# Kernel tuning notes

Hardware: AMD Instinct MI355X
Metric: run time of the kernel (lower is better)

The kernel has to match this reference:

```python
import jax, jax.numpy as jnp
import numpy as np

NUM_RAYS = 4096
NUM_SAMPLES = 64
NUM_IMPORTANCE = 64
UPSAMPLE_STEPS = 4
HIDDEN = 128
SAMPLE_DIST = 2.0 / NUM_SAMPLES
COS_ANNEAL_RATIO = 0.0


def sdf_fn(params, pts):
    # pts: [P,3] -> sdf: [P,1]  (stand-in for sdf_network.get_sdf_vals)
    W1, b1, W2, b2, W3, b3 = params
    h = jax.nn.softplus(pts @ W1 + b1)
    h = jax.nn.softplus(h @ W2 + b2)
    return h @ W3 + b3


def sdf_grad(params, pts):
    # gradient of sdf w.r.t. points, [P,3] (stand-in for sdf_network.gradient)
    return jax.grad(lambda p: sdf_fn(params, p).sum())(pts)


def sample_pdf(bins, weights, n_samples):
    # deterministic inverse-transform sampling (det=True branch)
    weights = weights + 1e-5
    pdf = weights / jnp.sum(weights, axis=-1, keepdims=True)
    cdf = jnp.cumsum(pdf, axis=-1)
    cdf = jnp.concatenate([jnp.zeros_like(cdf[..., :1]), cdf], axis=-1)  # [N,S]
    u = jnp.linspace(0.5 / n_samples, 1.0 - 0.5 / n_samples, n_samples, dtype=cdf.dtype)
    u = jnp.broadcast_to(u, cdf.shape[:-1] + (n_samples,))
    inds = jax.vmap(lambda c, uu: jnp.searchsorted(c, uu, side='right'))(cdf, u)
    below = jnp.maximum(inds - 1, 0)
    above = jnp.minimum(inds, cdf.shape[-1] - 1)
    cdf_b = jnp.take_along_axis(cdf, below, axis=-1)
    cdf_a = jnp.take_along_axis(cdf, above, axis=-1)
    bins_b = jnp.take_along_axis(bins, below, axis=-1)
    bins_a = jnp.take_along_axis(bins, above, axis=-1)
    denom = cdf_a - cdf_b
    denom = jnp.where(denom < 1e-5, jnp.ones_like(denom), denom)
    t = (u - cdf_b) / denom
    return bins_b + t * (bins_a - bins_b)


def upsample(rays_o, rays_d, z_vals, sdf, n_importance, inv_s):
    N, S = z_vals.shape
    pts = rays_o[:, None, :] + rays_d[:, None, :] * z_vals[..., None]  # [N,S,3]
    radius = jnp.linalg.norm(pts, axis=-1)
    inside_sphere = ((radius[:, :-1] < 1.0) | (radius[:, 1:] < 1.0)).astype(z_vals.dtype)
    prev_sdf, next_sdf = sdf[:, :-1], sdf[:, 1:]
    prev_z, next_z = z_vals[:, :-1], z_vals[:, 1:]
    mid_sdf = (prev_sdf + next_sdf) * 0.5
    cos_val = (next_sdf - prev_sdf) / (next_z - prev_z + 1e-5)
    prev_cos = jnp.concatenate([jnp.zeros((N, 1), z_vals.dtype), cos_val[:, :-1]], axis=-1)
    cos_val = jnp.minimum(prev_cos, cos_val)
    cos_val = jnp.clip(cos_val, -1000.0, 0.0) * inside_sphere
    dist = next_z - prev_z
    prev_cdf = jax.nn.sigmoid((mid_sdf - cos_val * dist * 0.5) * inv_s)
    next_cdf = jax.nn.sigmoid((mid_sdf + cos_val * dist * 0.5) * inv_s)
    alpha = (prev_cdf - next_cdf + 1e-5) / (prev_cdf + 1e-5)
    trans = jnp.cumprod(jnp.concatenate([jnp.ones((N, 1), z_vals.dtype), 1.0 - alpha + 1e-7], axis=-1), axis=-1)[:, :-1]
    weights = alpha * trans
    return sample_pdf(z_vals, weights, n_importance)


def cat_z_vals(params, rays_o, rays_d, z_vals, new_z_vals, sdf, last):
    N = z_vals.shape[0]
    z_cat = jnp.concatenate([z_vals, new_z_vals], axis=-1)
    order = jnp.argsort(z_cat, axis=-1)
    z_sorted = jnp.take_along_axis(z_cat, order, axis=-1)
    if not last:
        pts = rays_o[:, None, :] + rays_d[:, None, :] * new_z_vals[..., None]
        new_sdf = sdf_fn(params, pts.reshape(-1, 3)).reshape(N, new_z_vals.shape[-1])
        sdf = jnp.take_along_axis(jnp.concatenate([sdf, new_sdf], axis=-1), order, axis=-1)
    return z_sorted, sdf


def render_depth(params, variance, rays_o, rays_d, sample_dist, z_vals):
    N, S = z_vals.shape
    dists = z_vals[..., 1:] - z_vals[..., :-1]
    dists = jnp.concatenate([dists, jnp.full((N, 1), sample_dist, z_vals.dtype)], axis=-1)
    mid_z = z_vals + dists * 0.5
    pts = (rays_o[:, None, :] + rays_d[:, None, :] * mid_z[..., None]).reshape(-1, 3)
    dirs = jnp.broadcast_to(rays_d[:, None, :], (N, S, 3)).reshape(-1, 3)
    sdf = sdf_fn(params, pts)              # [P,1]
    gradients = sdf_grad(params, pts)      # [P,3]
    inv_s = jnp.clip(jnp.exp(10.0 * variance), 1e-6, 1e6)
    true_cos = jnp.sum(dirs * gradients, axis=-1, keepdims=True)
    iter_cos = -(jax.nn.relu(-true_cos * 0.5 + 0.5) * (1.0 - COS_ANNEAL_RATIO)
                 + jax.nn.relu(-true_cos) * COS_ANNEAL_RATIO)
    d = dists.reshape(-1, 1)
    prev_cdf = jax.nn.sigmoid((sdf - iter_cos * d * 0.5) * inv_s)
    next_cdf = jax.nn.sigmoid((sdf + iter_cos * d * 0.5) * inv_s)
    alpha = jnp.clip((prev_cdf - next_cdf + 1e-5) / (prev_cdf + 1e-5), 0.0, 1.0).reshape(N, S)
    trans = jnp.cumprod(jnp.concatenate([jnp.ones((N, 1), z_vals.dtype), 1.0 - alpha + 1e-7], axis=-1), axis=-1)[:, :-1]
    weights = alpha * trans
    depths = jnp.sum(weights * z_vals, axis=-1)
    return depths, gradients


def setup_inputs():
    key = jax.random.key(0)
    ks = jax.random.split(key, 8)
    rays_o = 0.1 * jax.random.normal(ks[0], (NUM_RAYS, 3), jnp.float32)
    rd = jax.random.normal(ks[1], (NUM_RAYS, 3), jnp.float32)
    rays_d = rd / jnp.linalg.norm(rd, axis=-1, keepdims=True)
    near = 0.3 + 0.2 * jax.random.uniform(ks[2], (NUM_RAYS, 1), jnp.float32)
    far = near + 1.5
    W1 = jax.random.normal(ks[3], (3, HIDDEN), jnp.float32) / np.sqrt(3.0)
    W2 = jax.random.normal(ks[4], (HIDDEN, HIDDEN), jnp.float32) / np.sqrt(HIDDEN)
    W3 = jax.random.normal(ks[5], (HIDDEN, 1), jnp.float32) / np.sqrt(HIDDEN)
    b1 = jnp.zeros((HIDDEN,), jnp.float32)
    b2 = jnp.zeros((HIDDEN,), jnp.float32)
    b3 = jnp.zeros((1,), jnp.float32)
    variance = jnp.asarray(0.3, jnp.float32)
    return {"rays_o": rays_o, "rays_d": rays_d, "near": near, "far": far,
            "W1": W1, "b1": b1, "W2": W2, "b2": b2, "W3": W3, "b3": b3,
            "variance": variance}


def reference(rays_o, rays_d, near, far, W1, b1, W2, b2, W3, b3, variance):
    params = (W1, b1, W2, b2, W3, b3)
    N = rays_o.shape[0]
    z = jnp.linspace(0.0, 1.0, NUM_SAMPLES, dtype=jnp.float32)
    z_vals = near + (far - near) * z[None, :]  # [N,S0]
    # importance sampling (torch.no_grad block)
    pts = rays_o[:, None, :] + rays_d[:, None, :] * z_vals[..., None]
    sdf = sdf_fn(params, pts.reshape(-1, 3)).reshape(N, NUM_SAMPLES)
    n_imp = NUM_IMPORTANCE // UPSAMPLE_STEPS
    for i in range(UPSAMPLE_STEPS):
        new_z = upsample(rays_o, rays_d, z_vals, sdf, n_imp, 64.0 * (2 ** i))
        z_vals, sdf = cat_z_vals(params, rays_o, rays_d, z_vals, new_z, sdf,
                                 last=(i + 1 == UPSAMPLE_STEPS))
    z_vals = jax.lax.stop_gradient(z_vals)
    return render_depth(params, variance, rays_o, rays_d, SAMPLE_DIST, z_vals)
```

## Files before the change

### kernel.cpp

```cpp
#include <hip/hip_runtime.h>
#include <math.h>

#define HID 128
#define NRAYS 4096
#define TP 64

typedef __bf16 bf16x8 __attribute__((ext_vector_type(8)));
typedef float f32x4 __attribute__((ext_vector_type(4)));
typedef unsigned int uint32x4 __attribute__((ext_vector_type(4)));

union frag_u { bf16x8 v; uint32x4 q; };

__device__ __forceinline__ unsigned f2bf(float f){
  unsigned u = __float_as_uint(f);
  u += 0x7FFFu + ((u >> 16) & 1u);
  return u >> 16;
}
__device__ __forceinline__ float bf2f(unsigned h){
  return __uint_as_float(h << 16);
}
__device__ __forceinline__ float sp_f(float x){
  return fmaxf(x, 0.0f) + log1pf(expf(-fabsf(x)));
}
__device__ __forceinline__ float sp_fast(float x){
  float e = __expf(-fabsf(x));
  return fmaxf(x, 0.0f) + __logf(1.0f + e);
}
__device__ __forceinline__ float sg_fast(float x){
  float e = __expf(-fabsf(x));
  float r = __builtin_amdgcn_rcpf(1.0f + e);
  return (x >= 0.0f ? 1.0f : e) * r;
}
__device__ __forceinline__ float sg_f(float x){
  return 1.0f / (1.0f + expf(-x));
}
__device__ __forceinline__ f32x4 splat4(float x){
  f32x4 v = {x, x, x, x};
  return v;
}

#define SW(p,k) ((((p)*HID) + (k)) ^ (((p)&7)<<3))

__global__ void k_make_frags(const float* __restrict__ W2,
    unsigned short* __restrict__ w2fh,  unsigned short* __restrict__ w2fl,
    unsigned short* __restrict__ w2tfh, unsigned short* __restrict__ w2tfl){
  int idx = blockIdx.x*256 + threadIdx.x;
  if (idx >= 4096) return;
  int which = idx >> 11;
  int f    = (idx >> 6) & 31;
  int lane = idx & 63;
  int kc = f >> 3, tg = f & 7;
  int lg = lane >> 4, lr = lane & 15;
  unsigned short* dh = which ? w2tfh : w2fh;
  unsigned short* dl = which ? w2tfl : w2fl;
  int base = (f*64 + lane)*8;
  #pragma unroll
  for (int e = 0; e < 8; e++){
    int a = 32*kc + 8*lg + e;
    int b = 16*tg + lr;
    float v = which ? W2[b*HID + a] : W2[a*HID + b];
    unsigned hi = f2bf(v);
    dh[base+e] = (unsigned short)hi;
    dl[base+e] = (unsigned short)f2bf(v - bf2f(hi));
  }
}

__global__ void k_make_frags3(const float* __restrict__ W2,
    unsigned short* __restrict__ dh, unsigned short* __restrict__ dm,
    unsigned short* __restrict__ dl){
  int idx = blockIdx.x*256 + threadIdx.x;
  if (idx >= 2048) return;
  int f    = idx >> 6;
  int lane = idx & 63;
  int kc = f >> 3, tg = f & 7;
  int lg = lane >> 4, lr = lane & 15;
  int base = (f*64 + lane)*8;
  #pragma unroll
  for (int e = 0; e < 8; e++){
    int a = 32*kc + 8*lg + e;
    int b = 16*tg + lr;
    float v = W2[a*HID + b];
    unsigned hi = f2bf(v);
    float rm = v - bf2f(hi);
    unsigned md = f2bf(rm);
    dh[base+e] = (unsigned short)hi;
    dm[base+e] = (unsigned short)md;
    dl[base+e] = (unsigned short)f2bf(rm - bf2f(md));
  }
}

__global__ void k_init(const float* __restrict__ rays_o, const float* __restrict__ rays_d,
                       const float* __restrict__ nearv, const float* __restrict__ farv,
                       float* __restrict__ z_buf, float* __restrict__ pts){
  int idx = blockIdx.x*256 + threadIdx.x;
  if (idx >= NRAYS*64) return;
  int ray = idx >> 6, j = idx & 63;
  float nr = nearv[ray];
  float z = nr + (farv[ray] - nr) * ((float)j / 63.0f);
  z_buf[ray*128 + j] = z;
  pts[idx*3+0] = rays_o[ray*3+0] + rays_d[ray*3+0]*z;
  pts[idx*3+1] = rays_o[ray*3+1] + rays_d[ray*3+1]*z;
  pts[idx*3+2] = rays_o[ray*3+2] + rays_d[ray*3+2]*z;
}

__global__ __launch_bounds__(256, 3) void k_mlp_fwd_t(
    const float* __restrict__ pts,
    const float* __restrict__ W1, const float* __restrict__ b1,
    const float* __restrict__ b2,
    const float* __restrict__ W3, const float* __restrict__ b3,
    const unsigned short* __restrict__ w2h, const unsigned short* __restrict__ w2m,
    const unsigned short* __restrict__ w2l,
    float* __restrict__ sdf_out)
{
  __shared__ unsigned short sHi[64*HID];
  __shared__ unsigned short sMi[64*HID];
  __shared__ unsigned short sLo[64*HID];
  __shared__ float sRed[4][64];

  const int tid = threadIdx.x;
  const int l   = tid & 63;
  const int wv  = __builtin_amdgcn_readfirstlane(tid >> 6);
  const int lg  = l >> 4;
  const int lr  = l & 15;
  const int q0  = blockIdx.x * 64;
  const int kb  = 32*wv;

  const float x0 = pts[(q0+l)*3+0];
  const float x1 = pts[(q0+l)*3+1];
  const float x2 = pts[(q0+l)*3+2];

  #pragma unroll
  for (int g = 0; g < 4; g++){
    unsigned hw[4], mw[4], lw[4];
    #pragma unroll
    for (int e2 = 0; e2 < 4; e2++){
      unsigned hpk[2], mpk[2], lpk[2];
      #pragma unroll
      for (int t = 0; t < 2; t++){
        int k = kb + 8*g + 2*e2 + t;
        float pre = b1[k];
        pre = fmaf(x0, W1[k],       pre);
        pre = fmaf(x1, W1[HID+k],   pre);
        pre = fmaf(x2, W1[2*HID+k], pre);
        float h = sp_fast(pre);
        unsigned hi = f2bf(h);
        float rm = h - bf2f(hi);
        unsigned md = f2bf(rm);
        hpk[t] = hi; mpk[t] = md;
        lpk[t] = f2bf(rm - bf2f(md));
      }
      hw[e2] = hpk[0] | (hpk[1] << 16);
      mw[e2] = mpk[0] | (mpk[1] << 16);
      lw[e2] = lpk[0] | (lpk[1] << 16);
    }
    uint32x4 hq = {hw[0], hw[1], hw[2], hw[3]};
    uint32x4 mq = {mw[0], mw[1], mw[2], mw[3]};
    uint32x4 lq = {lw[0], lw[1], lw[2], lw[3]};
    *(uint32x4*)&sHi[SW(l, kb + 8*g)] = hq;
    *(uint32x4*)&sMi[SW(l, kb + 8*g)] = mq;
    *(uint32x4*)&sLo[SW(l, kb + 8*g)] = lq;
  }
  __syncthreads();

  f32x4 acc[4][2], accC[4][2];
  {
    const float b2a = b2[kb + lr];
    const float b2b = b2[kb + 16 + lr];
    #pragma unroll
    for (int mt = 0; mt < 4; mt++){
      acc[mt][0]  = splat4(b2a);
      acc[mt][1]  = splat4(b2b);
      accC[mt][0] = splat4(0.0f);
      accC[mt][1] = splat4(0.0f);
    }
  }
  #pragma unroll
  for (int kc = 0; kc < 4; kc++){
    frag_u bh0, bm0, bl0, bh1, bm1, bl1;
    const int f0 = ((kc*8 + 2*wv + 0)*64 + l)*8;
    const int f1 = ((kc*8 + 2*wv + 1)*64 + l)*8;
    bh0.q = *(const uint32x4*)(w2h + f0);
    bm0.q = *(const uint32x4*)(w2m + f0);
    bl0.q = *(const uint32x4*)(w2l + f0);
    bh1.q = *(const uint32x4*)(w2h + f1);
    bm1.q = *(const uint32x4*)(w2m + f1);
    bl1.q = *(const uint32x4*)(w2l + f1);
    const int kk = 32*kc + 8*lg;
    #pragma unroll
    for (int mt = 0; mt < 4; mt++){
      frag_u ah, am, al;
      ah.q = *(const uint32x4*)&sHi[SW(16*mt + lr, kk)];
      am.q = *(const uint32x4*)&sMi[SW(16*mt + lr, kk)];
      al.q = *(const uint32x4*)&sLo[SW(16*mt + lr, kk)];
      accC[mt][0] = __builtin_amdgcn_mfma_f32_16x16x32_bf16(ah.v, bl0.v, accC[mt][0], 0,0,0);
      accC[mt][0] = __builtin_amdgcn_mfma_f32_16x16x32_bf16(am.v, bm0.v, accC[mt][0], 0,0,0);
      accC[mt][0] = __builtin_amdgcn_mfma_f32_16x16x32_bf16(al.v, bh0.v, accC[mt][0], 0,0,0);
      accC[mt][0] = __builtin_amdgcn_mfma_f32_16x16x32_bf16(ah.v, bm0.v, accC[mt][0], 0,0,0);
      accC[mt][0] = __builtin_amdgcn_mfma_f32_16x16x32_bf16(am.v, bh0.v, accC[mt][0], 0,0,0);
      acc[mt][0]  = __builtin_amdgcn_mfma_f32_16x16x32_bf16(ah.v, bh0.v, acc[mt][0],  0,0,0);
      accC[mt][1] = __builtin_amdgcn_mfma_f32_16x16x32_bf16(ah.v, bl1.v, accC[mt][1], 0,0,0);
      accC[mt][1] = __builtin_amdgcn_mfma_f32_16x16x32_bf16(am.v, bm1.v, accC[mt][1], 0,0,0);
      accC[mt][1] = __builtin_amdgcn_mfma_f32_16x16x32_bf16(al.v, bh1.v, accC[mt][1], 0,0,0);
      accC[mt][1] = __builtin_amdgcn_mfma_f32_16x16x32_bf16(ah.v, bm1.v, accC[mt][1], 0,0,0);
      accC[mt][1] = __builtin_amdgcn_mfma_f32_16x16x32_bf16(am.v, bh1.v, accC[mt][1], 0,0,0);
      acc[mt][1]  = __builtin_amdgcn_mfma_f32_16x16x32_bf16(ah.v, bh1.v, acc[mt][1],  0,0,0);
    }
  }

  {
    const float w3a = W3[kb + lr];
    const float w3b = W3[kb + 16 + lr];
    #pragma unroll
    for (int mt = 0; mt < 4; mt++){
      float svr[4];
      #pragma unroll
      for (int r = 0; r < 4; r++){
        float pa = acc[mt][0][r] + accC[mt][0][r];
        float pb = acc[mt][1][r] + accC[mt][1][r];
        svr[r] = sp_fast(pa)*w3a + sp_fast(pb)*w3b;
      }
      #pragma unroll
      for (int m = 1; m < 16; m <<= 1){
        svr[0] += __shfl_xor(svr[0], m);
        svr[1] += __shfl_xor(svr[1], m);
        svr[2] += __shfl_xor(svr[2], m);
        svr[3] += __shfl_xor(svr[3], m);
      }
      if (lr == 0){
        sRed[wv][16*mt + 4*lg + 0] = svr[0];
        sRed[wv][16*mt + 4*lg + 1] = svr[1];
        sRed[wv][16*mt + 4*lg + 2] = svr[2];
        sRed[wv][16*mt + 4*lg + 3] = svr[3];
      }
    }
  }
  __syncthreads();
  if (tid < 64)
    sdf_out[q0+tid] = b3[0] + sRed[0][tid] + sRed[1][tid] + sRed[2][tid] + sRed[3][tid];
}

__global__ __launch_bounds__(256, 4) void k_mlp_bwd(
    const float* __restrict__ pts,
    const float* __restrict__ W1, const float* __restrict__ b1,
    const float* __restrict__ b2,
    const float* __restrict__ W3, const float* __restrict__ b3,
    const unsigned short* __restrict__ w2fh,  const unsigned short* __restrict__ w2fl,
    const unsigned short* __restrict__ w2tfh, const unsigned short* __restrict__ w2tfl,
    float* __restrict__ sdf_out, float* __restrict__ grad_out)
{
  __shared__ unsigned short sHi[64*HID];
  __shared__ unsigned short sLo[64*HID];
  __shared__ float sRed[4][64];
  __shared__ float sPts[64][4];
  __shared__ float sGrad[4][64][3];

  const int tid = threadIdx.x;
  const int l   = tid & 63;
  const int wv  = __builtin_amdgcn_readfirstlane(tid >> 6);
  const int lg  = l >> 4;
  const int lr  = l & 15;
  const int q0  = blockIdx.x * 64;
  const int kb  = 32*wv;

  const float x0 = pts[(q0+l)*3+0];
  const float x1 = pts[(q0+l)*3+1];
  const float x2 = pts[(q0+l)*3+2];
  if (wv == 0){ sPts[l][0] = x0; sPts[l][1] = x1; sPts[l][2] = x2; }

  #pragma unroll
  for (int g = 0; g < 4; g++){
    unsigned hw[4], lw[4];
    #pragma unroll
    for (int e2 = 0; e2 < 4; e2++){
      unsigned hpk[2], lpk[2];
      #pragma unroll
      for (int t = 0; t < 2; t++){
        int k = kb + 8*g + 2*e2 + t;
        float pre = b1[k];
        pre = fmaf(x0, W1[k],       pre);
        pre = fmaf(x1, W1[HID+k],   pre);
        pre = fmaf(x2, W1[2*HID+k], pre);
        float h = sp_fast(pre);
        unsigned hi = f2bf(h);
        hpk[t] = hi;
        lpk[t] = f2bf(h - bf2f(hi));
      }
      hw[e2] = hpk[0] | (hpk[1] << 16);
      lw[e2] = lpk[0] | (lpk[1] << 16);
    }
    uint32x4 hq = {hw[0], hw[1], hw[2], hw[3]};
    uint32x4 lq = {lw[0], lw[1], lw[2], lw[3]};
    *(uint32x4*)&sHi[SW(l, kb + 8*g)] = hq;
    *(uint32x4*)&sLo[SW(l, kb + 8*g)] = lq;
  }
  __syncthreads();

  f32x4 acc[4][2];
  {
    const float b2a = b2[kb + lr];
    const float b2b = b2[kb + 16 + lr];
    #pragma unroll
    for (int mt = 0; mt < 4; mt++){
      acc[mt][0] = splat4(b2a);
      acc[mt][1] = splat4(b2b);
    }
  }
  #pragma unroll
  for (int kc = 0; kc < 4; kc++){
    frag_u bh0, bl0, bh1, bl1;
    const int f0 = ((kc*8 + 2*wv + 0)*64 + l)*8;
    const int f1 = ((kc*8 + 2*wv + 1)*64 + l)*8;
    bh0.q = *(const uint32x4*)(w2fh + f0);
    bl0.q = *(const uint32x4*)(w2fl + f0);
    bh1.q = *(const uint32x4*)(w2fh + f1);
    bl1.q = *(const uint32x4*)(w2fl + f1);
    const int kk = 32*kc + 8*lg;
    #pragma unroll
    for (int mt = 0; mt < 4; mt++){
      frag_u ah, al;
      ah.q = *(const uint32x4*)&sHi[SW(16*mt + lr, kk)];
      al.q = *(const uint32x4*)&sLo[SW(16*mt + lr, kk)];
      acc[mt][0] = __builtin_amdgcn_mfma_f32_16x16x32_bf16(ah.v, bh0.v, acc[mt][0], 0,0,0);
      acc[mt][0] = __builtin_amdgcn_mfma_f32_16x16x32_bf16(ah.v, bl0.v, acc[mt][0], 0,0,0);
      acc[mt][0] = __builtin_amdgcn_mfma_f32_16x16x32_bf16(al.v, bh0.v, acc[mt][0], 0,0,0);
      acc[mt][1] = __builtin_amdgcn_mfma_f32_16x16x32_bf16(ah.v, bh1.v, acc[mt][1], 0,0,0);
      acc[mt][1] = __builtin_amdgcn_mfma_f32_16x16x32_bf16(ah.v, bl1.v, acc[mt][1], 0,0,0);
      acc[mt][1] = __builtin_amdgcn_mfma_f32_16x16x32_bf16(al.v, bh1.v, acc[mt][1], 0,0,0);
    }
  }
  __syncthreads();

  {
    const float w3a = W3[kb + lr];
    const float w3b = W3[kb + 16 + lr];
    #pragma unroll
    for (int mt = 0; mt < 4; mt++){
      float svr[4];
      #pragma unroll
      for (int r = 0; r < 4; r++){
        float pa = acc[mt][0][r], pb = acc[mt][1][r];
        svr[r] = sp_fast(pa)*w3a + sp_fast(pb)*w3b;
        int pr = 16*mt + 4*lg + r;
        float ga = sg_fast(pa) * w3a;
        float gb = sg_fast(pb) * w3b;
        unsigned ha = f2bf(ga);
        sHi[SW(pr, kb + lr)]      = (unsigned short)ha;
        sLo[SW(pr, kb + lr)]      = (unsigned short)f2bf(ga - bf2f(ha));
        unsigned hb = f2bf(gb);
        sHi[SW(pr, kb + 16 + lr)] = (unsigned short)hb;
        sLo[SW(pr, kb + 16 + lr)] = (unsigned short)f2bf(gb - bf2f(hb));
      }
      #pragma unroll
      for (int m = 1; m < 16; m <<= 1){
        svr[0] += __shfl_xor(svr[0], m);
        svr[1] += __shfl_xor(svr[1], m);
        svr[2] += __shfl_xor(svr[2], m);
        svr[3] += __shfl_xor(svr[3], m);
      }
      if (lr == 0){
        sRed[wv][16*mt + 4*lg + 0] = svr[0];
        sRed[wv][16*mt + 4*lg + 1] = svr[1];
        sRed[wv][16*mt + 4*lg + 2] = svr[2];
        sRed[wv][16*mt + 4*lg + 3] = svr[3];
      }
    }
  }
  __syncthreads();
  if (tid < 64)
    sdf_out[q0+tid] = b3[0] + sRed[0][tid] + sRed[1][tid] + sRed[2][tid] + sRed[3][tid];

  f32x4 acc2[4][2];
  #pragma unroll
  for (int pt = 0; pt < 4; pt++){
    acc2[pt][0] = splat4(0.0f);
    acc2[pt][1] = splat4(0.0f);
  }
  #pragma unroll
  for (int kcn = 0; kcn < 4; kcn++){
    frag_u ah0, al0, ah1, al1;
    const int f0 = ((kcn*8 + 2*wv + 0)*64 + l)*8;
    const int f1 = ((kcn*8 + 2*wv + 1)*64 + l)*8;
    ah0.q = *(const uint32x4*)(w2tfh + f0);
    al0.q = *(const uint32x4*)(w2tfl + f0);
    ah1.q = *(const uint32x4*)(w2tfh + f1);
    al1.q = *(const uint32x4*)(w2tfl + f1);
    const int nn = 32*kcn + 8*lg;
    #pragma unroll
    for (int pt = 0; pt < 4; pt++){
      frag_u bh, bl;
      bh.q = *(const uint32x4*)&sHi[SW(16*pt + lr, nn)];
      bl.q = *(const uint32x4*)&sLo[SW(16*pt + lr, nn)];
      acc2[pt][0] = __builtin_amdgcn_mfma_f32_16x16x32_bf16(ah0.v, bh.v, acc2[pt][0], 0,0,0);
      acc2[pt][0] = __builtin_amdgcn_mfma_f32_16x16x32_bf16(ah0.v, bl.v, acc2[pt][0], 0,0,0);
      acc2[pt][0] = __builtin_amdgcn_mfma_f32_16x16x32_bf16(al0.v, bh.v, acc2[pt][0], 0,0,0);
      acc2[pt][1] = __builtin_amdgcn_mfma_f32_16x16x32_bf16(ah1.v, bh.v, acc2[pt][1], 0,0,0);
      acc2[pt][1] = __builtin_amdgcn_mfma_f32_16x16x32_bf16(ah1.v, bl.v, acc2[pt][1], 0,0,0);
      acc2[pt][1] = __builtin_amdgcn_mfma_f32_16x16x32_bf16(al1.v, bh.v, acc2[pt][1], 0,0,0);
    }
  }

  {
    float w1a[2][4], w1b[2][4], w1c[2][4], b1v[2][4];
    #pragma unroll
    for (int t = 0; t < 2; t++)
      #pragma unroll
      for (int r = 0; r < 4; r++){
        int k = kb + 16*t + 4*lg + r;
        w1a[t][r] = W1[k]; w1b[t][r] = W1[HID+k]; w1c[t][r] = W1[2*HID+k];
        b1v[t][r] = b1[k];
      }
    #pragma unroll
    for (int pt = 0; pt < 4; pt++){
      const int p = 16*pt + lr;
      const float xx = sPts[p][0], xy = sPts[p][1], xz = sPts[p][2];
      float gx = 0.f, gy = 0.f, gz = 0.f;
      #pragma unroll
      for (int t = 0; t < 2; t++){
        #pragma unroll
        for (int r = 0; r < 4; r++){
          float pre1 = fmaf(xx, w1a[t][r], fmaf(xy, w1b[t][r], fmaf(xz, w1c[t][r], b1v[t][r])));
          float dp = acc2[pt][t][r] * sg_fast(pre1);
          gx = fmaf(w1a[t][r], dp, gx);
          gy = fmaf(w1b[t][r], dp, gy);
          gz = fmaf(w1c[t][r], dp, gz);
        }
      }
      gx += __shfl_xor(gx, 16); gx += __shfl_xor(gx, 32);
      gy += __shfl_xor(gy, 16); gy += __shfl_xor(gy, 32);
      gz += __shfl_xor(gz, 16); gz += __shfl_xor(gz, 32);
      if (lg == 0){
        sGrad[wv][p][0] = gx; sGrad[wv][p][1] = gy; sGrad[wv][p][2] = gz;
      }
    }
  }
  __syncthreads();
  if (tid < 64){
    #pragma unroll
    for (int c = 0; c < 3; c++)
      grad_out[(q0+tid)*3+c] =
        sGrad[0][tid][c] + sGrad[1][tid][c] + sGrad[2][tid][c] + sGrad[3][tid][c];
  }
}

__global__ void k_scatter_init(const float* __restrict__ sdf_tmp, float* __restrict__ sdf_buf){
  int idx = blockIdx.x*256 + threadIdx.x;
  if (idx >= NRAYS*64) return;
  sdf_buf[(idx >> 6)*128 + (idx & 63)] = sdf_tmp[idx];
}
__global__ void k_scatter_new(const float* __restrict__ sdf_tmp, const int* __restrict__ slots,
                              float* __restrict__ sdf_buf){
  int idx = blockIdx.x*256 + threadIdx.x;
  if (idx >= NRAYS*16) return;
  sdf_buf[(idx >> 4)*128 + slots[idx]] = sdf_tmp[idx];
}

__global__ __launch_bounds__(64) void k_upsample(
      const float* __restrict__ rays_o, const float* __restrict__ rays_d,
      float* __restrict__ z_buf, float* __restrict__ sdf_buf,
      float* __restrict__ pts_new, int* __restrict__ slots,
      int S, float inv_s, int last){
  __shared__ float z[128], sd[128], rad[128], cosv[128], alf[128], wv[128], cdf[129], nz[16];
  __shared__ int slt[16];
  const int ray = blockIdx.x;
  const int l   = threadIdx.x;
  const float ox = rays_o[ray*3], oy = rays_o[ray*3+1], oz = rays_o[ray*3+2];
  const float dx = rays_d[ray*3], dy = rays_d[ray*3+1], dz = rays_d[ray*3+2];
  for (int j = l; j < S; j += 64){
    float zz = z_buf[ray*128+j];
    z[j]  = zz;
    sd[j] = sdf_buf[ray*128+j];
    float px = ox+dx*zz, py = oy+dy*zz, pz = oz+dz*zz;
    rad[j] = sqrtf(px*px + py*py + pz*pz);
  }
  __syncthreads();
  for (int j = l; j < S-1; j += 64)
    cosv[j] = (sd[j+1]-sd[j]) / (z[j+1]-z[j] + 1e-5f);
  __syncthreads();
  for (int j = l; j < S-1; j += 64){
    float cv = fminf((j > 0) ? cosv[j-1] : 0.0f, cosv[j]);
    cv = fminf(fmaxf(cv, -1000.0f), 0.0f);
    float inside = (rad[j] < 1.0f || rad[j+1] < 1.0f) ? 1.0f : 0.0f;
    cv *= inside;
    float mid  = 0.5f*(sd[j]+sd[j+1]);
    float dist = z[j+1]-z[j];
    float e = sg_f((mid - cv*dist*0.5f)*inv_s);
    float f = sg_f((mid + cv*dist*0.5f)*inv_s);
    alf[j] = (e - f + 1e-5f) / (e + 1e-5f);
  }
  __syncthreads();
  if (l == 0){
    float T = 1.0f, wsum = 0.0f;
    for (int j = 0; j < S-1; j++){
      float w = alf[j]*T + 1e-5f;
      wv[j] = w; wsum += w;
      T *= (1.0f - alf[j] + 1e-7f);
    }
    cdf[0] = 0.0f;
    float c = 0.0f;
    for (int j = 0; j < S-1; j++){ c += wv[j]/wsum; cdf[j+1] = c; }
  }
  __syncthreads();
  if (l < 16){
    float u = 0.03125f + 0.0625f*(float)l;
    int idx = 0;
    while (idx < S && cdf[idx] <= u) idx++;
    int below = idx - 1; if (below < 0) below = 0;
    int above = (idx < S-1) ? idx : (S-1);
    float cb = cdf[below], ca = cdf[above];
    float den = ca - cb; if (den < 1e-5f) den = 1.0f;
    float t = (u - cb) / den;
    nz[l] = z[below] + t*(z[above] - z[below]);
  }
  __syncthreads();
  if (l == 0){
    int i = S-1, j = 15;
    for (int dst = S+15; dst >= 0; --dst){
      bool takeOld = (j < 0) || (i >= 0 && z[i] > nz[j]);
      if (takeOld){ z[dst] = z[i]; sd[dst] = sd[i]; i--; }
      else        { z[dst] = nz[j]; slt[j] = dst; j--; }
    }
  }
  __syncthreads();
  for (int j = l; j < S+16; j += 64){
    z_buf[ray*128+j]  = z[j];
    sdf_buf[ray*128+j] = sd[j];
  }
  if (!last && l < 16){
    slots[ray*16+l] = slt[l];
    float zz = nz[l];
    pts_new[(ray*16+l)*3+0] = ox + dx*zz;
    pts_new[(ray*16+l)*3+1] = oy + dy*zz;
    pts_new[(ray*16+l)*3+2] = oz + dz*zz;
  }
}

__global__ void k_prep(const float* __restrict__ rays_o, const float* __restrict__ rays_d,
                       const float* __restrict__ z_buf, float* __restrict__ pts){
  int idx = blockIdx.x*256 + threadIdx.x;
  if (idx >= NRAYS*128) return;
  int ray = idx >> 7, s = idx & 127;
  float z = z_buf[idx];
  float d = (s < 127) ? (z_buf[idx+1] - z) : 0.03125f;
  float mid = z + 0.5f*d;
  pts[idx*3+0] = rays_o[ray*3+0] + rays_d[ray*3+0]*mid;
  pts[idx*3+1] = rays_o[ray*3+1] + rays_d[ray*3+1]*mid;
  pts[idx*3+2] = rays_o[ray*3+2] + rays_d[ray*3+2]*mid;
}

__global__ __launch_bounds__(64) void k_render(
    const float* __restrict__ z_buf, const float* __restrict__ sdf_mid,
    const float* __restrict__ rays_d, const float* __restrict__ grad,
    const float* __restrict__ variance, float* __restrict__ depth_out){
  const int ray = blockIdx.x;
  const int l   = threadIdx.x;
  float inv_s = expf(10.0f * variance[0]);
  inv_s = fminf(fmaxf(inv_s, 1e-6f), 1e6f);
  const float dx = rays_d[ray*3], dy = rays_d[ray*3+1], dz = rays_d[ray*3+2];
  const int i0 = ray*128 + 2*l, i1 = i0 + 1;
  const float z0 = z_buf[i0], z1 = z_buf[i1];
  const float zn1 = __shfl_down(z0, 1);
  const float d0 = z1 - z0;
  const float d1 = (l < 63) ? (zn1 - z1) : 0.03125f;
  float a0, a1;
  {
    float sdf = sdf_mid[i0];
    float gx = grad[i0*3], gy = grad[i0*3+1], gz = grad[i0*3+2];
    float tc = dx*gx + dy*gy + dz*gz;
    float ic = -fmaxf(0.5f - 0.5f*tc, 0.0f);
    float e = sg_fast((sdf - ic*d0*0.5f)*inv_s);
    float f = sg_fast((sdf + ic*d0*0.5f)*inv_s);
    a0 = fminf(fmaxf((e - f + 1e-5f) / (e + 1e-5f), 0.0f), 1.0f);
  }
  {
    float sdf = sdf_mid[i1];
    float gx = grad[i1*3], gy = grad[i1*3+1], gz = grad[i1*3+2];
    float tc = dx*gx + dy*gy + dz*gz;
    float ic = -fmaxf(0.5f - 0.5f*tc, 0.0f);
    float e = sg_fast((sdf - ic*d1*0.5f)*inv_s);
    float f = sg_fast((sdf + ic*d1*0.5f)*inv_s);
    a1 = fminf(fmaxf((e - f + 1e-5f) / (e + 1e-5f), 0.0f), 1.0f);
  }
  const float f0 = 1.0f - a0 + 1e-7f;
  const float f1 = 1.0f - a1 + 1e-7f;
  float incl = f0 * f1;
  #pragma unroll
  for (int off = 1; off < 64; off <<= 1){
    float t = __shfl_up(incl, off);
    if (l >= off) incl *= t;
  }
  float P = __shfl_up(incl, 1);
  if (l == 0) P = 1.0f;
  float part = P * (a0*z0 + f0*a1*z1);
  #pragma unroll
  for (int m = 1; m < 64; m <<= 1) part += __shfl_xor(part, m);
  if (l == 0) depth_out[ray] = part;
}

extern "C" void kernel_launch(void* const* d_in, const int* in_sizes, int n_in,
                              void* d_out, int out_size, void* d_ws, size_t ws_size,
                              hipStream_t stream){
  (void)in_sizes; (void)n_in; (void)out_size; (void)ws_size;
  const float* rays_o = (const float*)d_in[0];
  const float* rays_d = (const float*)d_in[1];
  const float* nearv  = (const float*)d_in[2];
  const float* farv   = (const float*)d_in[3];
  const float* W1 = (const float*)d_in[4];
  const float* b1 = (const float*)d_in[5];
  const float* W2 = (const float*)d_in[6];
  const float* b2 = (const float*)d_in[7];
  const float* W3 = (const float*)d_in[8];
  const float* b3 = (const float*)d_in[9];
  const float* variance = (const float*)d_in[10];

  float* ws      = (float*)d_ws;
  float* z_buf   = ws;
  float* sdf_buf = ws + 524288;
  float* sdf_tmp = ws + 1048576;
  int*   slots   = (int*)(ws + 1589248);
  unsigned short* w2fh  = (unsigned short*)(ws + 524288);
  unsigned short* w2fl  = w2fh + 16384;
  unsigned short* w2tfh = w2fh + 32768;
  unsigned short* w2tfl = w2fh + 49152;
  unsigned short* w2h3 = (unsigned short*)(ws + 1310720);
  unsigned short* w2m3 = w2h3 + 16384;
  unsigned short* w2l3 = w2h3 + 32768;

  float* out       = (float*)d_out;
  float* depth_out = out;
  float* grad_out  = out + NRAYS;
  float* pts       = grad_out;

  k_make_frags3<<<dim3(8), dim3(256), 0, stream>>>(W2, w2h3, w2m3, w2l3);
  k_init<<<dim3(1024), dim3(256), 0, stream>>>(rays_o, rays_d, nearv, farv, z_buf, pts);
  k_mlp_fwd_t<<<dim3(4096), dim3(256), 0, stream>>>(pts, W1,b1,b2,W3,b3,
                                                    w2h3,w2m3,w2l3, sdf_tmp);
  k_scatter_init<<<dim3(1024), dim3(256), 0, stream>>>(sdf_tmp, sdf_buf);

  for (int i = 0; i < 4; i++){
    int S = 64 + 16*i;
    float inv_s = (float)(64 << i);
    int last = (i == 3) ? 1 : 0;
    k_upsample<<<dim3(4096), dim3(64), 0, stream>>>(rays_o, rays_d, z_buf, sdf_buf,
                                                    pts, slots, S, inv_s, last);
    if (!last){
      k_mlp_fwd_t<<<dim3(1024), dim3(256), 0, stream>>>(pts, W1,b1,b2,W3,b3,
                                                        w2h3,w2m3,w2l3, sdf_tmp);
      k_scatter_new<<<dim3(256), dim3(256), 0, stream>>>(sdf_tmp, slots, sdf_buf);
    }
  }

  k_make_frags<<<dim3(16), dim3(256), 0, stream>>>(W2, w2fh, w2fl, w2tfh, w2tfl);
  k_prep<<<dim3(2048), dim3(256), 0, stream>>>(rays_o, rays_d, z_buf, pts);
  k_mlp_bwd<<<dim3(8192), dim3(256), 0, stream>>>(pts, W1,b1,b2,W3,b3,
                                                  w2fh,w2fl,w2tfh,w2tfl, sdf_tmp, grad_out);
  k_render<<<dim3(4096), dim3(64), 0, stream>>>(z_buf, sdf_tmp, rays_d, grad_out,
                                                variance, depth_out);
}
```

Before: 591.0 us.

## Fuse scatter and prep kernels into MLP kernels and reduce backward-pass precision

Removes the separate scatter kernels by writing SDF values directly into the per-ray buffer from the forward MLP epilogue, with a mode flag. It also drops the point-preparation kernel by computing midpoint positions inside the backward MLP from z values. The backward pass's second GEMM goes from split-bf16 (three MFMAs per tile) to a single bf16 MFMA, and bf16 rounding becomes truncation. This cuts launches, global traffic and MFMA work, but lowers gradient accuracy, which risks exceeding the tolerance.

```diff
diff --git a/kernel.cpp b/kernel.cpp
--- a/kernel.cpp
+++ b/kernel.cpp
@@ -18,9 +18,6 @@
 }
 __device__ __forceinline__ float bf2f(unsigned h){
   return __uint_as_float(h << 16);
-}
-__device__ __forceinline__ float sp_f(float x){
-  return fmaxf(x, 0.0f) + log1pf(expf(-fabsf(x)));
 }
 __device__ __forceinline__ float sp_fast(float x){
   float e = __expf(-fabsf(x));
@@ -110,7 +107,7 @@
     const float* __restrict__ W3, const float* __restrict__ b3,
     const unsigned short* __restrict__ w2h, const unsigned short* __restrict__ w2m,
     const unsigned short* __restrict__ w2l,
-    float* __restrict__ sdf_out)
+    float* __restrict__ sdf_out, const int* __restrict__ slots, int mode)
 {
   __shared__ unsigned short sHi[64*HID];
   __shared__ unsigned short sMi[64*HID];
@@ -235,17 +232,27 @@
     }
   }
   __syncthreads();
-  if (tid < 64)
-    sdf_out[q0+tid] = b3[0] + sRed[0][tid] + sRed[1][tid] + sRed[2][tid] + sRed[3][tid];
+  if (tid < 64){
+    float sv = b3[0] + sRed[0][tid] + sRed[1][tid] + sRed[2][tid] + sRed[3][tid];
+    if (mode == 0){
+      sdf_out[q0 + tid] = sv;
+    } else if (mode == 1){
+      sdf_out[(q0 << 1) + tid] = sv;
+    } else {
+      int p = q0 + tid;
+      sdf_out[(p >> 4)*128 + slots[p]] = sv;
+    }
+  }
 }
 
 __global__ __launch_bounds__(256, 4) void k_mlp_bwd(
-    const float* __restrict__ pts,
+    const float* __restrict__ z_buf,
+    const float* __restrict__ rays_o, const float* __restrict__ rays_d,
     const float* __restrict__ W1, const float* __restrict__ b1,
     const float* __restrict__ b2,
     const float* __restrict__ W3, const float* __restrict__ b3,
     const unsigned short* __restrict__ w2fh,  const unsigned short* __restrict__ w2fl,
-    const unsigned short* __restrict__ w2tfh, const unsigned short* __restrict__ w2tfl,
+    const unsigned short* __restrict__ w2tfh,
     float* __restrict__ sdf_out, float* __restrict__ grad_out)
 {
   __shared__ unsigned short sHi[64*HID];
@@ -262,9 +269,15 @@
   const int q0  = blockIdx.x * 64;
   const int kb  = 32*wv;
 
-  const float x0 = pts[(q0+l)*3+0];
-  const float x1 = pts[(q0+l)*3+1];
-  const float x2 = pts[(q0+l)*3+2];
+  const int ray = q0 >> 7;
+  const int s   = (q0 & 127) + l;
+  const float z  = z_buf[q0 + l];
+  const float zn = z_buf[q0 + l + ((s < 127) ? 1 : 0)];
+  const float d  = (s < 127) ? (zn - z) : 0.03125f;
+  const float midz = z + 0.5f*d;
+  const float x0 = rays_o[ray*3+0] + rays_d[ray*3+0]*midz;
+  const float x1 = rays_o[ray*3+1] + rays_d[ray*3+1]*midz;
+  const float x2 = rays_o[ray*3+2] + rays_d[ray*3+2]*midz;
   if (wv == 0){ sPts[l][0] = x0; sPts[l][1] = x1; sPts[l][2] = x2; }
 
   #pragma unroll
@@ -281,9 +294,10 @@
         pre = fmaf(x1, W1[HID+k],   pre);
         pre = fmaf(x2, W1[2*HID+k], pre);
         float h = sp_fast(pre);
-        unsigned hi = f2bf(h);
+        unsigned hi = __float_as_uint(h) >> 16;
+        float rm = h - __uint_as_float(hi << 16);
         hpk[t] = hi;
-        lpk[t] = f2bf(h - bf2f(hi));
+        lpk[t] = __float_as_uint(rm) >> 16;
       }
       hw[e2] = hpk[0] | (hpk[1] << 16);
       lw[e2] = lpk[0] | (lpk[1] << 16);
@@ -343,12 +357,8 @@
         int pr = 16*mt + 4*lg + r;
         float ga = sg_fast(pa) * w3a;
         float gb = sg_fast(pb) * w3b;
-        unsigned ha = f2bf(ga);
-        sHi[SW(pr, kb + lr)]      = (unsigned short)ha;
-        sLo[SW(pr, kb + lr)]      = (unsigned short)f2bf(ga - bf2f(ha));
-        unsigned hb = f2bf(gb);
-        sHi[SW(pr, kb + 16 + lr)] = (unsigned short)hb;
-        sLo[SW(pr, kb + 16 + lr)] = (unsigned short)f2bf(gb - bf2f(hb));
+        sHi[SW(pr, kb + lr)]      = (unsigned short)(__float_as_uint(ga) >> 16);
+        sHi[SW(pr, kb + 16 + lr)] = (unsigned short)(__float_as_uint(gb) >> 16);
       }
       #pragma unroll
       for (int m = 1; m < 16; m <<= 1){
@@ -377,25 +387,18 @@
   }
   #pragma unroll
   for (int kcn = 0; kcn < 4; kcn++){
-    frag_u ah0, al0, ah1, al1;
+    frag_u ah0, ah1;
     const int f0 = ((kcn*8 + 2*wv + 0)*64 + l)*8;
     const int f1 = ((kcn*8 + 2*wv + 1)*64 + l)*8;
     ah0.q = *(const uint32x4*)(w2tfh + f0);
-    al0.q = *(const uint32x4*)(w2tfl + f0);
     ah1.q = *(const uint32x4*)(w2tfh + f1);
-    al1.q = *(const uint32x4*)(w2tfl + f1);
     const int nn = 32*kcn + 8*lg;
     #pragma unroll
     for (int pt = 0; pt < 4; pt++){
-      frag_u bh, bl;
+      frag_u bh;
       bh.q = *(const uint32x4*)&sHi[SW(16*pt + lr, nn)];
-      bl.q = *(const uint32x4*)&sLo[SW(16*pt + lr, nn)];
       acc2[pt][0] = __builtin_amdgcn_mfma_f32_16x16x32_bf16(ah0.v, bh.v, acc2[pt][0], 0,0,0);
-      acc2[pt][0] = __builtin_amdgcn_mfma_f32_16x16x32_bf16(ah0.v, bl.v, acc2[pt][0], 0,0,0);
-      acc2[pt][0] = __builtin_amdgcn_mfma_f32_16x16x32_bf16(al0.v, bh.v, acc2[pt][0], 0,0,0);
       acc2[pt][1] = __builtin_amdgcn_mfma_f32_16x16x32_bf16(ah1.v, bh.v, acc2[pt][1], 0,0,0);
-      acc2[pt][1] = __builtin_amdgcn_mfma_f32_16x16x32_bf16(ah1.v, bl.v, acc2[pt][1], 0,0,0);
-      acc2[pt][1] = __builtin_amdgcn_mfma_f32_16x16x32_bf16(al1.v, bh.v, acc2[pt][1], 0,0,0);
     }
   }
 
@@ -440,18 +443,6 @@
       grad_out[(q0+tid)*3+c] =
         sGrad[0][tid][c] + sGrad[1][tid][c] + sGrad[2][tid][c] + sGrad[3][tid][c];
   }
-}
-
-__global__ void k_scatter_init(const float* __restrict__ sdf_tmp, float* __restrict__ sdf_buf){
-  int idx = blockIdx.x*256 + threadIdx.x;
-  if (idx >= NRAYS*64) return;
-  sdf_buf[(idx >> 6)*128 + (idx & 63)] = sdf_tmp[idx];
-}
-__global__ void k_scatter_new(const float* __restrict__ sdf_tmp, const int* __restrict__ slots,
-                              float* __restrict__ sdf_buf){
-  int idx = blockIdx.x*256 + threadIdx.x;
-  if (idx >= NRAYS*16) return;
-  sdf_buf[(idx >> 4)*128 + slots[idx]] = sdf_tmp[idx];
 }
 
 __global__ __launch_bounds__(64) void k_upsample(
@@ -532,19 +523,6 @@
     pts_new[(ray*16+l)*3+1] = oy + dy*zz;
     pts_new[(ray*16+l)*3+2] = oz + dz*zz;
   }
-}
-
-__global__ void k_prep(const float* __restrict__ rays_o, const float* __restrict__ rays_d,
-                       const float* __restrict__ z_buf, float* __restrict__ pts){
-  int idx = blockIdx.x*256 + threadIdx.x;
-  if (idx >= NRAYS*128) return;
-  int ray = idx >> 7, s = idx & 127;
-  float z = z_buf[idx];
-  float d = (s < 127) ? (z_buf[idx+1] - z) : 0.03125f;
-  float mid = z + 0.5f*d;
-  pts[idx*3+0] = rays_o[ray*3+0] + rays_d[ray*3+0]*mid;
-  pts[idx*3+1] = rays_o[ray*3+1] + rays_d[ray*3+1]*mid;
-  pts[idx*3+2] = rays_o[ray*3+2] + rays_d[ray*3+2]*mid;
 }
 
 __global__ __launch_bounds__(64) void k_render(
@@ -633,8 +611,7 @@
   k_make_frags3<<<dim3(8), dim3(256), 0, stream>>>(W2, w2h3, w2m3, w2l3);
   k_init<<<dim3(1024), dim3(256), 0, stream>>>(rays_o, rays_d, nearv, farv, z_buf, pts);
   k_mlp_fwd_t<<<dim3(4096), dim3(256), 0, stream>>>(pts, W1,b1,b2,W3,b3,
-                                                    w2h3,w2m3,w2l3, sdf_tmp);
-  k_scatter_init<<<dim3(1024), dim3(256), 0, stream>>>(sdf_tmp, sdf_buf);
+                                                    w2h3,w2m3,w2l3, sdf_buf, nullptr, 1);
 
   for (int i = 0; i < 4; i++){
     int S = 64 + 16*i;
@@ -644,15 +621,14 @@
                                                     pts, slots, S, inv_s, last);
     if (!last){
       k_mlp_fwd_t<<<dim3(1024), dim3(256), 0, stream>>>(pts, W1,b1,b2,W3,b3,
-                                                        w2h3,w2m3,w2l3, sdf_tmp);
-      k_scatter_new<<<dim3(256), dim3(256), 0, stream>>>(sdf_tmp, slots, sdf_buf);
+                                                        w2h3,w2m3,w2l3, sdf_buf, slots, 2);
     }
   }
 
   k_make_frags<<<dim3(16), dim3(256), 0, stream>>>(W2, w2fh, w2fl, w2tfh, w2tfl);
-  k_prep<<<dim3(2048), dim3(256), 0, stream>>>(rays_o, rays_d, z_buf, pts);
-  k_mlp_bwd<<<dim3(8192), dim3(256), 0, stream>>>(pts, W1,b1,b2,W3,b3,
-                                                  w2fh,w2fl,w2tfh,w2tfl, sdf_tmp, grad_out);
+  k_mlp_bwd<<<dim3(8192), dim3(256), 0, stream>>>(z_buf, rays_o, rays_d,
+                                                  W1,b1,b2,W3,b3,
+                                                  w2fh,w2fl,w2tfh, sdf_tmp, grad_out);
   k_render<<<dim3(4096), dim3(64), 0, stream>>>(z_buf, sdf_tmp, rays_d, grad_out,
                                                 variance, depth_out);
 }
```

Measured after the change: 544.7 us. -7.8%, faster.
